# Kernel tuning notes

Hardware: AMD Instinct MI355X
Metric: run time of the kernel (lower is better)

The kernel has to match this reference:

```python
import jax, jax.numpy as jnp
import numpy as np

DIM = 1024
HEADS = 16
HEAD_DIM = 64
INNER = HEADS * HEAD_DIM  # 1024
B, N = 4, 2048
EPS = 1e-5


def setup_inputs() -> dict:
    key = jax.random.key(0)
    ks = jax.random.split(key, 5)
    x = jax.random.normal(ks[0], (B, N, DIM), dtype=jnp.float32)
    w_qkv = jax.random.normal(ks[1], (DIM, 3 * INNER), dtype=jnp.float32) * (DIM ** -0.5)
    w_out = jax.random.normal(ks[2], (INNER, DIM), dtype=jnp.float32) * (INNER ** -0.5)
    b_out = jax.random.normal(ks[3], (DIM,), dtype=jnp.float32) * 0.01
    ln_gamma = jnp.ones((DIM,), dtype=jnp.float32)
    ln_beta = jnp.zeros((DIM,), dtype=jnp.float32)
    return {"x": x, "w_qkv": w_qkv, "w_out": w_out, "b_out": b_out,
            "ln_gamma": ln_gamma, "ln_beta": ln_beta}


def reference(x, w_qkv, w_out, b_out, ln_gamma, ln_beta):
    scale = HEAD_DIM ** -0.5
    qkv = x @ w_qkv  # [b, n, 3*inner]
    q, k, v = jnp.split(qkv, 3, axis=-1)
    q = q * scale
    # [b, n, h*d] -> [b, h, n, d]
    def to_heads(t):
        b, n, _ = t.shape
        return t.reshape(b, n, HEADS, HEAD_DIM).transpose(0, 2, 1, 3)
    q, k, v = to_heads(q), to_heads(k), to_heads(v)
    scores = jnp.einsum('bhid,bhjd->bhij', q, k)
    attn = jax.nn.softmax(scores, axis=-1)  # max-subtraction (detached) is internal
    out = jnp.einsum('bhij,bhjd->bhid', attn, v)
    out = out.transpose(0, 2, 1, 3).reshape(x.shape[0], x.shape[1], INNER)
    out = out @ w_out + b_out
    # LayerNorm over last dim
    mu = out.mean(axis=-1, keepdims=True)
    var = out.var(axis=-1, keepdims=True)
    out = (out - mu) * jax.lax.rsqrt(var + EPS)
    return out * ln_gamma + ln_beta
```

## Files before the change

### kernel.cpp

```cpp
#include <hip/hip_runtime.h>


typedef __bf16 bf16;
typedef __bf16 bf16x4 __attribute__((ext_vector_type(4)));
typedef __bf16 bf16x8 __attribute__((ext_vector_type(8)));
typedef float f32x4 __attribute__((ext_vector_type(4)));
typedef float f32x16 __attribute__((ext_vector_type(16)));
typedef unsigned int u32x2 __attribute__((ext_vector_type(2)));
typedef unsigned int u32x4 __attribute__((ext_vector_type(4)));

#define QSCALE_LOG2E 0.18033688011112042f

#define GLOAD_LDS16(gp, lp)                                                   \
  __builtin_amdgcn_global_load_lds(                                           \
      (const __attribute__((address_space(1))) unsigned int*)(const void*)(gp), \
      (__attribute__((address_space(3))) unsigned int*)(void*)(lp), 16, 0, 0)

__device__ __forceinline__ float fexp2(float x) {
#if __has_builtin(__builtin_amdgcn_exp2f)
  return __builtin_amdgcn_exp2f(x);
#else
  return __expf(x * 0.6931471805599453f);
#endif
}

__device__ __forceinline__ unsigned pack2t(float lo, float hi) {
  return __builtin_amdgcn_perm(__float_as_uint(hi), __float_as_uint(lo), 0x07060302u);
}

__global__ __launch_bounds__(256) void prep_k(const float* __restrict__ x,
                                              const float* __restrict__ w_qkv,
                                              const float* __restrict__ w_out,
                                              bf16* __restrict__ xbf,
                                              bf16* __restrict__ wqkvT,
                                              bf16* __restrict__ woutT) {
  __shared__ bf16 t[32][36];
  const int bid = blockIdx.x;
  if (bid < 4096) {
    const size_t i = ((size_t)bid * 256 + threadIdx.x) * 8;
    float4 a = *(const float4*)(x + i);
    float4 b = *(const float4*)(x + i + 4);
    bf16x8 o = {(bf16)a.x, (bf16)a.y, (bf16)a.z, (bf16)a.w,
                (bf16)b.x, (bf16)b.y, (bf16)b.z, (bf16)b.w};
    *(bf16x8*)(xbf + i) = o;
    return;
  }
  const float* in;
  bf16* outp;
  int Kd, Nd, n0, k0;
  if (bid < 4096 + 3072) {
    const int idx = bid - 4096;
    in = w_qkv; outp = wqkvT; Kd = 1024; Nd = 3072;
    n0 = (idx % 96) * 32; k0 = (idx / 96) * 32;
  } else {
    const int idx = bid - 7168;
    in = w_out; outp = woutT; Kd = 1024; Nd = 1024;
    n0 = (idx & 31) * 32; k0 = (idx >> 5) * 32;
  }
  const int r = threadIdx.x >> 3, c4 = (threadIdx.x & 7) * 4;
  float4 v = *(const float4*)(in + (size_t)(k0 + r) * Nd + n0 + c4);
  t[c4 + 0][r] = (bf16)v.x; t[c4 + 1][r] = (bf16)v.y;
  t[c4 + 2][r] = (bf16)v.z; t[c4 + 3][r] = (bf16)v.w;
  __syncthreads();
  bf16x4 o = *(const bf16x4*)&t[r][c4];
  *(bf16x4*)(outp + (size_t)(n0 + r) * Kd + k0 + c4) = o;
}

template <bool QKV>
__global__ __launch_bounds__(256) void gemm2(const bf16* __restrict__ A,
                                             const bf16* __restrict__ Bt,
                                             bf16* __restrict__ C,
                                             bf16* __restrict__ Vt) {
  __shared__ bf16 As[128][32];
  __shared__ bf16 Bs[128][32];
  const int tid = threadIdx.x;
  const int l = tid & 63, w = tid >> 6;
  const int g = l >> 4, q = l & 15;
  const int wm = w >> 1, wn = w & 1;
  const int m0 = blockIdx.x * 128, n0 = blockIdx.y * 128;
  const int lr = l >> 2, lc = (l & 3) * 8;

  f32x4 acc[4][4] = {};

  for (int k0 = 0; k0 < 1024; k0 += 32) {
    __syncthreads();
#pragma unroll
    for (int i = 0; i < 2; i++) {
      const int c = w + i * 4;
      GLOAD_LDS16(A + (size_t)(m0 + c * 16 + lr) * 1024 + k0 + lc, &As[c * 16][0]);
      GLOAD_LDS16(Bt + (size_t)(n0 + c * 16 + lr) * 1024 + k0 + lc, &Bs[c * 16][0]);
    }
    __syncthreads();

    bf16x8 af[4], bfr[4];
#pragma unroll
    for (int mi = 0; mi < 4; mi++)
      af[mi] = *(const bf16x8*)&As[wm * 64 + mi * 16 + q][g * 8];
#pragma unroll
    for (int ni = 0; ni < 4; ni++)
      bfr[ni] = *(const bf16x8*)&Bs[wn * 64 + ni * 16 + q][g * 8];
#pragma unroll
    for (int mi = 0; mi < 4; mi++)
#pragma unroll
      for (int ni = 0; ni < 4; ni++)
        acc[mi][ni] = __builtin_amdgcn_mfma_f32_16x16x32_bf16(af[mi], bfr[ni], acc[mi][ni], 0, 0, 0);
  }

  if (QKV && n0 >= 2048) {
#pragma unroll
    for (int mi = 0; mi < 4; mi++)
#pragma unroll
      for (int ni = 0; ni < 4; ni++) {
        const int vcol = n0 - 2048 + wn * 64 + ni * 16 + q;
        const int h = vcol >> 6, d = vcol & 63;
        const int t0 = m0 + wm * 64 + mi * 16 + g * 4;
        const int b = t0 >> 11, n = t0 & 2047;
        bf16x4 o = {(bf16)acc[mi][ni][0], (bf16)acc[mi][ni][1],
                    (bf16)acc[mi][ni][2], (bf16)acc[mi][ni][3]};
        *(bf16x4*)(Vt + ((size_t)(b * 16 + h) * 64 + d) * 2048 + n) = o;
      }
  } else {
    const int ldc = QKV ? 2048 : 1024;
    const float s = (QKV && n0 < 1024) ? QSCALE_LOG2E : 1.0f;
#pragma unroll
    for (int mi = 0; mi < 4; mi++)
#pragma unroll
      for (int ni = 0; ni < 4; ni++) {
        const int col = n0 + wn * 64 + ni * 16 + q;
#pragma unroll
        for (int r = 0; r < 4; r++) {
          const int row = m0 + wm * 64 + mi * 16 + g * 4 + r;
          C[(size_t)row * ldc + col] = (bf16)(acc[mi][ni][r] * s);
        }
      }
  }
}

__global__ __launch_bounds__(256, 3) void attn_k(const bf16* __restrict__ qk,
                                                 const bf16* __restrict__ vt,
                                                 bf16* __restrict__ aout) {
  __shared__ bf16 Ks[3][64][64];
  __shared__ bf16 Vs[2][64][64];
  const int tid = threadIdx.x;
  const int l = tid & 63, w = tid >> 6;
  const int q = l & 31, hi = l >> 5, q7 = q & 7;

  const int flat = blockIdx.x;
  const int logical = (flat & 7) * 128 + (flat >> 3);
  const int qt = logical & 15, bh = logical >> 4;
  const int h = bh & 15, b = bh >> 4;
  const int qbase = qt * 128 + w * 32;

  const bf16* Kg = qk + (size_t)(b * 2048) * 2048 + 1024 + h * 64;
  const bf16* Vg = vt + ((size_t)(b * 16 + h) * 64) * 2048;

  bf16x8 qf[4];
  {
    const bf16* Qr = qk + (size_t)(b * 2048 + qbase + q) * 2048 + h * 64 + hi * 8;
#pragma unroll
    for (int i = 0; i < 4; i++) qf[i] = *(const bf16x8*)(Qr + i * 16);
  }

  const int r0 = tid >> 3, sp0 = ((tid & 7) ^ (r0 & 7)) * 8;
  const int ub = (tid >> 6) << 9;
#define STAGE_K(buf, kt)                                                        \
  do {                                                                          \
    bf16* kd = &Ks[buf][0][0];                                                  \
    GLOAD_LDS16(Kg + (size_t)((kt) + r0) * 2048 + sp0, kd + ub);                \
    GLOAD_LDS16(Kg + (size_t)((kt) + 32 + r0) * 2048 + sp0, kd + 2048 + ub);    \
  } while (0)
#define STAGE_V(buf, kt)                                                        \
  do {                                                                          \
    bf16* vd = &Vs[buf][0][0];                                                  \
    GLOAD_LDS16(Vg + (size_t)r0 * 2048 + (kt) + sp0, vd + ub);                  \
    GLOAD_LDS16(Vg + (size_t)(32 + r0) * 2048 + (kt) + sp0, vd + 2048 + ub);    \
  } while (0)

#define QKT(buf, sA, sB)                                                        \
  do {                                                                          \
    const char* Kb_ = (const char*)&Ks[buf][0][0];                              \
    __builtin_amdgcn_s_setprio(1);                                              \
    {                                                                           \
      f32x16 a_ = {};                                                           \
      _Pragma("unroll")                                                         \
      for (int i = 0; i < 4; i++) {                                             \
        bf16x8 kf = *(const bf16x8*)(Kb_ + q * 128 + (((2 * i + hi) ^ q7) << 4));\
        a_ = __builtin_amdgcn_mfma_f32_32x32x16_bf16(kf, qf[i], a_, 0, 0, 0);   \
      }                                                                         \
      sA = a_;                                                                  \
    }                                                                           \
    {                                                                           \
      f32x16 a_ = {};                                                           \
      _Pragma("unroll")                                                         \
      for (int i = 0; i < 4; i++) {                                             \
        bf16x8 kf = *(const bf16x8*)(Kb_ + (32 + q) * 128 +                     \
                                     (((2 * i + hi) ^ q7) << 4));               \
        a_ = __builtin_amdgcn_mfma_f32_32x32x16_bf16(kf, qf[i], a_, 0, 0, 0);   \
      }                                                                         \
      sB = a_;                                                                  \
    }                                                                           \
    __builtin_amdgcn_s_setprio(0);                                              \
  } while (0)

  f32x16 oacc[2] = {};
  float lsA = 0.f, lsB = 0.f;

  STAGE_K(0, 0);
  STAGE_V(0, 0);
  STAGE_K(1, 64);
  asm volatile("s_waitcnt vmcnt(0)" ::: "memory");
  __builtin_amdgcn_sched_barrier(0);
  __builtin_amdgcn_s_barrier();

  f32x16 s0, s1;
  QKT(0, s0, s1);

  int kq = 1;
  int ksb = 2;
  int vcur = 0;
  for (int kt = 0; kt < 2048; kt += 64) {
    asm volatile("s_waitcnt vmcnt(0)" ::: "memory");
    __builtin_amdgcn_sched_barrier(0);
    __builtin_amdgcn_s_barrier();

    if (kt + 128 < 2048) STAGE_K(ksb, kt + 128);
    if (kt + 64 < 2048) STAGE_V(vcur ^ 1, kt + 64);

    f32x16 n0v, n1v;
    QKT(kq, n0v, n1v);

#pragma unroll
    for (int r = 0; r < 16; r++) { s0[r] = fexp2(s0[r]); lsA += s0[r]; }
#pragma unroll
    for (int r = 0; r < 16; r++) { s1[r] = fexp2(s1[r]); lsB += s1[r]; }

    bf16x8 pfrag[4];
#pragma unroll
    for (int ks = 0; ks < 2; ks++) {
      const unsigned a0 = pack2t(s0[8 * ks + 0], s0[8 * ks + 1]);
      const unsigned a1 = pack2t(s0[8 * ks + 2], s0[8 * ks + 3]);
      const unsigned b0 = pack2t(s0[8 * ks + 4], s0[8 * ks + 5]);
      const unsigned b1 = pack2t(s0[8 * ks + 6], s0[8 * ks + 7]);
      u32x2 w0 = __builtin_amdgcn_permlane32_swap(a0, b0, false, false);
      u32x2 w1 = __builtin_amdgcn_permlane32_swap(a1, b1, false, false);
      u32x4 bw = {w0[0], w1[0], w0[1], w1[1]};
      pfrag[ks] = __builtin_bit_cast(bf16x8, bw);
    }
#pragma unroll
    for (int ks = 0; ks < 2; ks++) {
      const unsigned a0 = pack2t(s1[8 * ks + 0], s1[8 * ks + 1]);
      const unsigned a1 = pack2t(s1[8 * ks + 2], s1[8 * ks + 3]);
      const unsigned b0 = pack2t(s1[8 * ks + 4], s1[8 * ks + 5]);
      const unsigned b1 = pack2t(s1[8 * ks + 6], s1[8 * ks + 7]);
      u32x2 w0 = __builtin_amdgcn_permlane32_swap(a0, b0, false, false);
      u32x2 w1 = __builtin_amdgcn_permlane32_swap(a1, b1, false, false);
      u32x4 bw = {w0[0], w1[0], w0[1], w1[1]};
      pfrag[2 + ks] = __builtin_bit_cast(bf16x8, bw);
    }

    const char* Vb = (const char*)&Vs[vcur][0][0];
    __builtin_amdgcn_s_setprio(1);
#pragma unroll
    for (int dblk = 0; dblk < 2; dblk++) {
      bf16x8 vfr[4];
#pragma unroll
      for (int t = 0; t < 4; t++)
        vfr[t] = *(const bf16x8*)(Vb + (dblk * 32 + q) * 128 + (((2 * t + hi) ^ q7) << 4));
#pragma unroll
      for (int t = 0; t < 4; t++)
        oacc[dblk] = __builtin_amdgcn_mfma_f32_32x32x16_bf16(vfr[t], pfrag[t],
                                                             oacc[dblk], 0, 0, 0);
    }
    __builtin_amdgcn_s_setprio(0);

    s0 = n0v; s1 = n1v;
    kq = (kq == 2) ? 0 : kq + 1;
    ksb = (ksb == 2) ? 0 : ksb + 1;
    vcur ^= 1;
  }

  float lsum = lsA + lsB;
  {
    u32x2 t2 = __builtin_amdgcn_permlane32_swap(__float_as_uint(lsum),
                                                __float_as_uint(lsum), false, false);
    lsum = __uint_as_float(t2[0]) + __uint_as_float(t2[1]);
  }
  const float inv = 1.f / lsum;
  bf16* orow = aout + (size_t)(b * 2048 + qbase + q) * 1024 + h * 64 + hi * 4;
#pragma unroll
  for (int dblk = 0; dblk < 2; dblk++)
#pragma unroll
    for (int rg = 0; rg < 4; rg++) {
      bf16x4 o = {(bf16)(oacc[dblk][4 * rg + 0] * inv), (bf16)(oacc[dblk][4 * rg + 1] * inv),
                  (bf16)(oacc[dblk][4 * rg + 2] * inv), (bf16)(oacc[dblk][4 * rg + 3] * inv)};
      *(bf16x4*)(orow + dblk * 32 + rg * 8) = o;
    }
#undef QKT
#undef STAGE_K
#undef STAGE_V
}

__global__ __launch_bounds__(256) void ln_k(const bf16* __restrict__ proj,
                                            const float* __restrict__ bo,
                                            const float* __restrict__ gam,
                                            const float* __restrict__ bet,
                                            float* __restrict__ out) {
  const int tid = threadIdx.x;
  const int l = tid & 63, w = tid >> 6;
  const int row = blockIdx.x * 4 + w;
  const int c0 = l * 16;

  bf16x8 p0 = *(const bf16x8*)(proj + (size_t)row * 1024 + c0);
  bf16x8 p1 = *(const bf16x8*)(proj + (size_t)row * 1024 + c0 + 8);
  float v[16];
#pragma unroll
  for (int j = 0; j < 8; j++) { v[j] = (float)p0[j]; v[8 + j] = (float)p1[j]; }
#pragma unroll
  for (int j = 0; j < 4; j++) {
    float4 bv = *(const float4*)(bo + c0 + j * 4);
    v[4 * j + 0] += bv.x; v[4 * j + 1] += bv.y;
    v[4 * j + 2] += bv.z; v[4 * j + 3] += bv.w;
  }
  float s = 0.f, ss = 0.f;
#pragma unroll
  for (int j = 0; j < 16; j++) { s += v[j]; ss += v[j] * v[j]; }
#pragma unroll
  for (int off = 32; off > 0; off >>= 1) {
    s += __shfl_xor(s, off);
    ss += __shfl_xor(ss, off);
  }
  const float mean = s * (1.f / 1024.f);
  const float var = ss * (1.f / 1024.f) - mean * mean;
  const float rs = rsqrtf(var + 1e-5f);
#pragma unroll
  for (int j = 0; j < 4; j++) {
    float4 gv = *(const float4*)(gam + c0 + j * 4);
    float4 btv = *(const float4*)(bet + c0 + j * 4);
    float4 o;
    o.x = (v[4 * j + 0] - mean) * rs * gv.x + btv.x;
    o.y = (v[4 * j + 1] - mean) * rs * gv.y + btv.y;
    o.z = (v[4 * j + 2] - mean) * rs * gv.z + btv.z;
    o.w = (v[4 * j + 3] - mean) * rs * gv.w + btv.w;
    *(float4*)(out + (size_t)row * 1024 + c0 + j * 4) = o;
  }
}

extern "C" void kernel_launch(void* const* d_in, const int* in_sizes, int n_in,
                              void* d_out, int out_size, void* d_ws, size_t ws_size,
                              hipStream_t stream) {
  const float* x      = (const float*)d_in[0];
  const float* w_qkv  = (const float*)d_in[1];
  const float* w_out  = (const float*)d_in[2];
  const float* b_out  = (const float*)d_in[3];
  const float* gamma  = (const float*)d_in[4];
  const float* beta   = (const float*)d_in[5];
  float* out = (float*)d_out;

  char* ws = (char*)d_ws;
  bf16* xbf   = (bf16*)(ws);
  bf16* wqkvT = (bf16*)(ws + 16777216);
  bf16* woutT = (bf16*)(ws + 23068672);
  bf16* qkbuf = (bf16*)(ws + 25165824);
  bf16* vt    = (bf16*)(ws + 58720256);
  bf16* aout  = xbf;
  bf16* proj  = vt;

  dim3 blk(256);
  prep_k<<<8192, blk, 0, stream>>>(x, w_qkv, w_out, xbf, wqkvT, woutT);
  gemm2<true><<<dim3(64, 24), blk, 0, stream>>>(xbf, wqkvT, qkbuf, vt);
  attn_k<<<1024, blk, 0, stream>>>(qkbuf, vt, aout);
  gemm2<false><<<dim3(64, 8), blk, 0, stream>>>(aout, woutT, proj, nullptr);
  ln_k<<<2048, blk, 0, stream>>>(proj, b_out, gamma, beta, out);
}
```

Before: 203.4 us.

## Rewrite GEMMs as 256x256-tile, 8-wave, double-buffered pipelined kernel with swizzled LDS

```diff
diff --git a/kernel.cpp b/kernel.cpp
--- a/kernel.cpp
+++ b/kernel.cpp
@@ -67,73 +67,147 @@
 }
 
 template <bool QKV>
-__global__ __launch_bounds__(256) void gemm2(const bf16* __restrict__ A,
-                                             const bf16* __restrict__ Bt,
-                                             bf16* __restrict__ C,
-                                             bf16* __restrict__ Vt) {
-  __shared__ bf16 As[128][32];
-  __shared__ bf16 Bs[128][32];
+__global__ __launch_bounds__(512, 2) void gemm8(const bf16* __restrict__ A,
+                                                const bf16* __restrict__ Bt,
+                                                bf16* __restrict__ C,
+                                                bf16* __restrict__ Vt) {
+  __shared__ bf16 As[2][256][64];
+  __shared__ bf16 Bs[2][256][64];
   const int tid = threadIdx.x;
-  const int l = tid & 63, w = tid >> 6;
-  const int g = l >> 4, q = l & 15;
-  const int wm = w >> 1, wn = w & 1;
-  const int m0 = blockIdx.x * 128, n0 = blockIdx.y * 128;
-  const int lr = l >> 2, lc = (l & 3) * 8;
-
-  f32x4 acc[4][4] = {};
-
-  for (int k0 = 0; k0 < 1024; k0 += 32) {
-    __syncthreads();
-#pragma unroll
-    for (int i = 0; i < 2; i++) {
-      const int c = w + i * 4;
-      GLOAD_LDS16(A + (size_t)(m0 + c * 16 + lr) * 1024 + k0 + lc, &As[c * 16][0]);
-      GLOAD_LDS16(Bt + (size_t)(n0 + c * 16 + lr) * 1024 + k0 + lc, &Bs[c * 16][0]);
-    }
-    __syncthreads();
-
-    bf16x8 af[4], bfr[4];
-#pragma unroll
-    for (int mi = 0; mi < 4; mi++)
-      af[mi] = *(const bf16x8*)&As[wm * 64 + mi * 16 + q][g * 8];
-#pragma unroll
-    for (int ni = 0; ni < 4; ni++)
-      bfr[ni] = *(const bf16x8*)&Bs[wn * 64 + ni * 16 + q][g * 8];
-#pragma unroll
-    for (int mi = 0; mi < 4; mi++)
-#pragma unroll
-      for (int ni = 0; ni < 4; ni++)
-        acc[mi][ni] = __builtin_amdgcn_mfma_f32_16x16x32_bf16(af[mi], bfr[ni], acc[mi][ni], 0, 0, 0);
+  const int l = tid & 63, wid = tid >> 6;
+  const int q = l & 15, g = l >> 4, q7 = q & 7;
+  const int wm = wid >> 2, wn = wid & 3;
+
+  const int nwg = (int)gridDim.x;
+  const int flat = (int)blockIdx.x;
+  const int swz = (flat & 7) * (nwg >> 3) + (flat >> 3);
+  const int m0 = (swz & 31) * 256, n0 = (swz >> 5) * 256;
+
+  const int srow0 = tid >> 3;
+  const int scol = ((tid & 7) ^ (srow0 & 7)) * 8;
+#define STAGE_HALF(buf, half, kt)                                               \
+  do {                                                                          \
+    const int mh_ = (half) >> 1;                                                \
+    const bf16* src_ = ((half) & 1)                                             \
+        ? Bt + (size_t)(n0 + mh_ * 128) * 1024                                  \
+        : A + (size_t)(m0 + mh_ * 128) * 1024;                                  \
+    bf16* dst_ = ((half) & 1) ? &Bs[buf][mh_ * 128][0] : &As[buf][mh_ * 128][0];\
+    GLOAD_LDS16(src_ + (size_t)srow0 * 1024 + (kt) + scol, dst_ + tid * 8);     \
+    GLOAD_LDS16(src_ + (size_t)(srow0 + 64) * 1024 + (kt) + scol,               \
+                dst_ + tid * 8 + 4096);                                         \
+  } while (0)
+
+  const char* Ab0 = (const char*)&As[0][0][0];
+  const char* Bb0 = (const char*)&Bs[0][0][0];
+  const int a0 = q * 128;
+  const int gc0 = (g << 4) ^ (q7 << 4);
+  const int gc1 = ((4 + g) << 4) ^ (q7 << 4);
+
+  f32x4 acc[8][4] = {};
+  bf16x8 afr[4][2], bfr[2][2];
+
+#define READ_A(AB, mh)                                                          \
+  do {                                                                          \
+    _Pragma("unroll")                                                           \
+    for (int mf = 0; mf < 4; mf++) {                                            \
+      afr[mf][0] = *(const bf16x8*)((AB) + (mh) * 8192 + mf * 2048 + a0 + gc0); \
+      afr[mf][1] = *(const bf16x8*)((AB) + (mh) * 8192 + mf * 2048 + a0 + gc1); \
+    }                                                                           \
+  } while (0)
+#define READ_B(BB, nh)                                                          \
+  do {                                                                          \
+    _Pragma("unroll")                                                           \
+    for (int nf = 0; nf < 2; nf++) {                                            \
+      bfr[nf][0] = *(const bf16x8*)((BB) + (nh) * 4096 + nf * 2048 + a0 + gc0); \
+      bfr[nf][1] = *(const bf16x8*)((BB) + (nh) * 4096 + nf * 2048 + a0 + gc1); \
+    }                                                                           \
+  } while (0)
+#define MMA(mh, nh)                                                             \
+  do {                                                                          \
+    __builtin_amdgcn_s_setprio(1);                                              \
+    _Pragma("unroll")                                                           \
+    for (int mf = 0; mf < 4; mf++)                                              \
+      _Pragma("unroll")                                                         \
+      for (int nf = 0; nf < 2; nf++)                                            \
+        _Pragma("unroll")                                                       \
+        for (int ks = 0; ks < 2; ks++)                                          \
+          acc[(mh) * 4 + mf][(nh) * 2 + nf] = __builtin_amdgcn_mfma_f32_16x16x32_bf16( \
+              afr[mf][ks], bfr[nf][ks], acc[(mh) * 4 + mf][(nh) * 2 + nf], 0, 0, 0);   \
+    __builtin_amdgcn_s_setprio(0);                                              \
+  } while (0)
+#define WAITBAR(N)                                                              \
+  do {                                                                          \
+    asm volatile("s_waitcnt vmcnt(" #N ")" ::: "memory");                       \
+    __builtin_amdgcn_sched_barrier(0);                                          \
+    __builtin_amdgcn_s_barrier();                                               \
+    __builtin_amdgcn_sched_barrier(0);                                          \
+  } while (0)
+
+  STAGE_HALF(0, 0, 0);
+  STAGE_HALF(0, 1, 0);
+  STAGE_HALF(0, 2, 0);
+  STAGE_HALF(0, 3, 0);
+
+  for (int t = 0; t < 16; ++t) {
+    const int bufo = (t & 1) * 32768;
+    const int nb = (t & 1) ^ 1;
+    const int kt1 = (t + 1) * 64;
+    const char* AB = Ab0 + bufo + wm * 16384;
+    const char* BB = Bb0 + bufo + wn * 8192;
+
+    WAITBAR(4);
+    STAGE_HALF(nb, 0, kt1);
+    READ_A(AB, 0);
+    READ_B(BB, 0);
+    MMA(0, 0);
+
+    WAITBAR(4);
+    STAGE_HALF(nb, 1, kt1);
+    READ_A(AB, 1);
+    MMA(1, 0);
+
+    WAITBAR(4);
+    STAGE_HALF(nb, 2, kt1);
+    READ_B(BB, 1);
+    MMA(1, 1);
+
+    STAGE_HALF(nb, 3, kt1);
+    READ_A(AB, 0);
+    MMA(0, 1);
   }
 
   if (QKV && n0 >= 2048) {
 #pragma unroll
-    for (int mi = 0; mi < 4; mi++)
-#pragma unroll
-      for (int ni = 0; ni < 4; ni++) {
-        const int vcol = n0 - 2048 + wn * 64 + ni * 16 + q;
+    for (int a = 0; a < 8; a++)
+#pragma unroll
+      for (int c = 0; c < 4; c++) {
+        const int vcol = n0 - 2048 + wn * 64 + (c >> 1) * 32 + (c & 1) * 16 + q;
         const int h = vcol >> 6, d = vcol & 63;
-        const int t0 = m0 + wm * 64 + mi * 16 + g * 4;
+        const int t0 = m0 + wm * 128 + (a >> 2) * 64 + (a & 3) * 16 + g * 4;
         const int b = t0 >> 11, n = t0 & 2047;
-        bf16x4 o = {(bf16)acc[mi][ni][0], (bf16)acc[mi][ni][1],
-                    (bf16)acc[mi][ni][2], (bf16)acc[mi][ni][3]};
+        bf16x4 o = {(bf16)acc[a][c][0], (bf16)acc[a][c][1],
+                    (bf16)acc[a][c][2], (bf16)acc[a][c][3]};
         *(bf16x4*)(Vt + ((size_t)(b * 16 + h) * 64 + d) * 2048 + n) = o;
       }
   } else {
     const int ldc = QKV ? 2048 : 1024;
     const float s = (QKV && n0 < 1024) ? QSCALE_LOG2E : 1.0f;
 #pragma unroll
-    for (int mi = 0; mi < 4; mi++)
-#pragma unroll
-      for (int ni = 0; ni < 4; ni++) {
-        const int col = n0 + wn * 64 + ni * 16 + q;
-#pragma unroll
-        for (int r = 0; r < 4; r++) {
-          const int row = m0 + wm * 64 + mi * 16 + g * 4 + r;
-          C[(size_t)row * ldc + col] = (bf16)(acc[mi][ni][r] * s);
-        }
+    for (int a = 0; a < 8; a++)
+#pragma unroll
+      for (int c = 0; c < 4; c++) {
+        const int col = n0 + wn * 64 + (c >> 1) * 32 + (c & 1) * 16 + q;
+        const int row0 = m0 + wm * 128 + (a >> 2) * 64 + (a & 3) * 16 + g * 4;
+#pragma unroll
+        for (int r = 0; r < 4; r++)
+          C[(size_t)(row0 + r) * ldc + col] = (bf16)(acc[a][c][r] * s);
       }
   }
+#undef WAITBAR
+#undef MMA
+#undef READ_B
+#undef READ_A
+#undef STAGE_HALF
 }
 
 __global__ __launch_bounds__(256, 3) void attn_k(const bf16* __restrict__ qk,
@@ -215,9 +289,7 @@
   f32x16 s0, s1;
   QKT(0, s0, s1);
 
-  int kq = 1;
-  int ksb = 2;
-  int vcur = 0;
+  int kq = 1, ksb = 2, vcur = 0;
   for (int kt = 0; kt < 2048; kt += 64) {
     asm volatile("s_waitcnt vmcnt(0)" ::: "memory");
     __builtin_amdgcn_sched_barrier(0);
@@ -367,8 +439,8 @@
 
   dim3 blk(256);
   prep_k<<<8192, blk, 0, stream>>>(x, w_qkv, w_out, xbf, wqkvT, woutT);
-  gemm2<true><<<dim3(64, 24), blk, 0, stream>>>(xbf, wqkvT, qkbuf, vt);
+  gemm8<true><<<384, dim3(512), 0, stream>>>(xbf, wqkvT, qkbuf, vt);
   attn_k<<<1024, blk, 0, stream>>>(qkbuf, vt, aout);
-  gemm2<false><<<dim3(64, 8), blk, 0, stream>>>(aout, woutT, proj, nullptr);
+  gemm8<false><<<128, dim3(512), 0, stream>>>(aout, woutT, proj, nullptr);
   ln_k<<<2048, blk, 0, stream>>>(proj, b_out, gamma, beta, out);
 }
```

New measurement: 256.9 us. +26.3%, slower.
